# Performance work log

Measured on AMD Instinct MI355X. Metric: run time of the kernel, lower is better.

Reference implementation:

```python
import jax, jax.numpy as jnp
import numpy as np

CONF_THRESH = 0.5   # foreground objectness threshold (module default)
NMS_THRESH = 0.4    # IoU suppression threshold (module default)
SCORE_THRESH = 0.3  # hard-coded max-class-score filter in forward

BS, NUM_BOXES, NUM_ATTRS = 2, 6300, 85  # 80 classes


def setup_inputs() -> dict:
    key = jax.random.key(0)
    # uniform [0,1): boxes live in the unit square and overlap heavily,
    # objectness/class scores frequently exceed the thresholds.
    x = jax.random.uniform(key, (BS, NUM_BOXES, NUM_ATTRS), dtype=jnp.float32)
    return {"x": x}


def _nms_keep(corners, scores, cls_idx, valid):
    """Per-image, per-class greedy NMS.

    corners: [N,4] (x1,y1,x2,y2), scores: [N] objectness, cls_idx: [N] int,
    valid: [N] bool. Returns keep mask [N] bool. Faithful to the torch loop:
    sort by objectness desc, greedily keep the top box of each class and
    suppress same-class boxes with IoU >= nms_thresh (torch keeps iou < t).
    """
    n = scores.shape[0]
    order = jnp.argsort(-scores)      # descending by objectness (column 4)
    rank = jnp.argsort(order)         # rank[j] = position of box j in order

    x1, y1, x2, y2 = corners[:, 0], corners[:, 1], corners[:, 2], corners[:, 3]
    area = (x2 - x1) * (y2 - y1)
    iw = jnp.maximum(jnp.minimum(x2[:, None], x2[None, :]) -
                     jnp.maximum(x1[:, None], x1[None, :]), 0.0)
    ih = jnp.maximum(jnp.minimum(y2[:, None], y2[None, :]) -
                     jnp.maximum(y1[:, None], y1[None, :]), 0.0)
    inter = iw * ih                                   # [N,N]
    iou = inter / (area[:, None] + area[None, :] - inter + 1e-16)
    same_cls = cls_idx[:, None] == cls_idx[None, :]    # [N,N]

    def body(r, keep):
        i = order[r]
        # suppress strictly lower-ranked, still-alive, same-class overlaps
        sup = (iou[i] >= NMS_THRESH) & same_cls[i] & (rank > r)
        return jnp.where(keep[i], keep & ~sup, keep)

    return jax.lax.fori_loop(0, n, body, valid)


def reference(x):
    """x: [bs, N, 5+num_classes]. Returns detections [bs, N, 8]:
    [batch_idx, x1, y1, x2, y2, p_obj, max_cls_score, cls_idx],
    zeroed for suppressed / filtered boxes (fixed-shape analogue of the
    variable-length torch output)."""
    conf_mask = x[..., 4] > CONF_THRESH
    xm = x * conf_mask[..., None].astype(x.dtype)

    # center -> corner transform
    xy, wh = xm[..., :2], xm[..., 2:4]
    corners = jnp.concatenate([xy - wh * 0.5, xy + wh * 0.5], axis=-1)  # [bs,N,4]

    p_obj = xm[..., 4]
    cls_scores = xm[..., 5:]
    max_score = jnp.max(cls_scores, axis=-1)
    cls_idx = jnp.argmax(cls_scores, axis=-1)
    valid = conf_mask & (max_score > SCORE_THRESH)

    keep = jax.vmap(_nms_keep)(corners, p_obj, cls_idx, valid)  # [bs,N] bool

    bs, n = p_obj.shape
    batch_idx = jnp.broadcast_to(
        jnp.arange(bs, dtype=x.dtype)[:, None], (bs, n))
    det = jnp.concatenate([
        batch_idx[..., None], corners, p_obj[..., None],
        max_score[..., None], cls_idx.astype(x.dtype)[..., None]], axis=-1)
    return det * keep[..., None].astype(x.dtype)
```

## Files before the change

### kernel.cpp

```cpp
#include <hip/hip_runtime.h>

#define BSZ    2
#define NBOX   6300
#define NATTR  85
#define NCLS   80
#define NREP   8
#define RCAP   64
#define CAP    256
#define POISON 0xAAAAAAAAu
#define NCC    (BSZ * NCLS)

typedef unsigned long long ull;

static __device__ __forceinline__ ull mask_for(int rem) {
  if (rem <= 0) return 0ull;
  if (rem >= 64) return ~0ull;
  return (1ull << rem) - 1ull;
}

__global__ __launch_bounds__(256) void prep_kernel(
    const float* __restrict__ x,
    unsigned int* __restrict__ ccount,
    int* __restrict__ clist,
    float* __restrict__ out) {
  int gid  = blockIdx.x * blockDim.x + threadIdx.x;
  int box  = gid >> 6;
  int lane = threadIdx.x & 63;
  int rep  = blockIdx.x & (NREP - 1);

  const float* p = x + (long)box * NATTR;
  float r0 = p[lane];
  float r1 = (lane < NATTR - 64) ? p[64 + lane] : -1.0f;

  float c0 = (lane >= 5) ? r0 : -1.0f;
  float v; int vi;
  if (r1 > c0) { v = r1; vi = 64 + lane; }
  else         { v = c0; vi = lane; }

  for (int off = 32; off > 0; off >>= 1) {
    float ov = __shfl_xor(v, off);
    int   oi = __shfl_xor(vi, off);
    if (ov > v || (ov == v && oi < vi)) { v = ov; vi = oi; }
  }

  float cx  = __shfl(r0, 0), cy = __shfl(r0, 1);
  float bw  = __shfl(r0, 2), bh = __shfl(r0, 3);
  float obj = __shfl(r0, 4);
  bool valid = (obj > 0.5f) && (v > 0.3f);
  int  img   = box >= NBOX ? 1 : 0;
  int  cls   = vi - 5;

  if (lane == 0) {
    float4 a, b;
    if (valid) {
      float hw = bw * 0.5f, hh = bh * 0.5f;
      a = make_float4((float)img, cx - hw, cy - hh, cx + hw);
      b = make_float4(cy + hh, obj, v, (float)cls);
      int cell = rep * NCC + img * NCLS + cls;
      unsigned int pos = atomicAdd(&ccount[cell], 1u) - POISON;
      if (pos < RCAP) clist[cell * RCAP + pos] = box - img * NBOX;
    } else {
      a = make_float4(0.f, 0.f, 0.f, 0.f);
      b = a;
    }
    float4* o = (float4*)(out + (long)box * 8);
    o[0] = a; o[1] = b;
  }
}

__global__ __launch_bounds__(64) void nms_kernel(
    const unsigned int* __restrict__ ccount,
    const int* __restrict__ clist,
    float* out) {
  __shared__ float ssc[CAP];
  __shared__ int   sbi[CAP];
  __shared__ float px1[CAP], py1[CAP], px2[CAP], py2[CAP];
  __shared__ int   pbi[CAP];

  int bc   = blockIdx.x;
  int img  = bc / NCLS;
  int lane = threadIdx.x;

  int cnt[NREP], off[NREP];
  int k = 0;
#pragma unroll
  for (int r = 0; r < NREP; r++) {
    unsigned int c = ccount[r * NCC + bc] - POISON;
    int ci = c > RCAP ? RCAP : (int)c;
    off[r] = k;
    k += ci;
    cnt[r] = ci;
  }
  if (k > CAP) k = CAP;
  if (k == 0) return;

  if (k <= 64) {
    float x1 = 0.f, y1 = 0.f, x2 = 0.f, y2 = 0.f, sc = 0.f;
    int bi = 0;
    if (lane < k) {
      int src = -1;
#pragma unroll
      for (int r = 0; r < NREP; r++)
        if (lane >= off[r] && lane < off[r] + cnt[r])
          src = (r * NCC + bc) * RCAP + (lane - off[r]);
      bi = clist[src];
      const float4* o = (const float4*)(out + ((long)img * NBOX + bi) * 8);
      float4 a = o[0], b = o[1];
      x1 = a.y; y1 = a.z; x2 = a.w; y2 = b.x; sc = b.y;
    }
    int rank = 0;
    for (int i = 0; i < k; i++) {
      float si  = __shfl(sc, i);
      int   bii = __shfl(bi, i);
      rank += (si > sc) || (si == sc && bii < bi);
    }
    if (lane >= k) rank = lane;

    int r4 = rank << 2;
    x1 = __int_as_float(__builtin_amdgcn_ds_permute(r4, __float_as_int(x1)));
    y1 = __int_as_float(__builtin_amdgcn_ds_permute(r4, __float_as_int(y1)));
    x2 = __int_as_float(__builtin_amdgcn_ds_permute(r4, __float_as_int(x2)));
    y2 = __int_as_float(__builtin_amdgcn_ds_permute(r4, __float_as_int(y2)));
    bi = __builtin_amdgcn_ds_permute(r4, bi);

    float ar = (x2 - x1) * (y2 - y1);

    ull keep = mask_for(k);
    for (int r = 0; r < k - 1; r++) {
      if (!((keep >> r) & 1ull)) continue;
      float X1 = __shfl(x1, r), Y1 = __shfl(y1, r);
      float X2 = __shfl(x2, r), Y2 = __shfl(y2, r);
      float AR = __shfl(ar, r);
      float iw = fminf(X2, x2) - fmaxf(X1, x1);
      float ih = fminf(Y2, y2) - fmaxf(Y1, y1);
      iw = fmaxf(iw, 0.0f); ih = fmaxf(ih, 0.0f);
      float inter = iw * ih;
      float iou = inter / (AR + ar - inter + 1e-16f);
      keep &= ~__ballot(iou >= 0.4f && lane > r);
    }

    if (lane < k && !((keep >> lane) & 1ull)) {
      float4 z = make_float4(0.f, 0.f, 0.f, 0.f);
      float4* o = (float4*)(out + ((long)img * NBOX + bi) * 8);
      o[0] = z; o[1] = z;
    }
    return;
  }

  float gx1[4], gy1[4], gx2[4], gy2[4], gsc[4];
  int   gbi[4];
#pragma unroll
  for (int s = 0; s < 4; s++) {
    int e = s * 64 + lane;
    gx1[s] = 0; gy1[s] = 0; gx2[s] = 0; gy2[s] = 0; gsc[s] = 0; gbi[s] = 0;
    if (e < k) {
      int src = -1;
#pragma unroll
      for (int r = 0; r < NREP; r++)
        if (e >= off[r] && e < off[r] + cnt[r])
          src = (r * NCC + bc) * RCAP + (e - off[r]);
      int bi = clist[src];
      const float4* o = (const float4*)(out + ((long)img * NBOX + bi) * 8);
      float4 a = o[0], b = o[1];
      gx1[s] = a.y; gy1[s] = a.z; gx2[s] = a.w; gy2[s] = b.x; gsc[s] = b.y;
      gbi[s] = bi;
      ssc[e] = b.y; sbi[e] = bi;
    }
  }
  __syncthreads();

#pragma unroll
  for (int s = 0; s < 4; s++) {
    int e = s * 64 + lane;
    if (e < k) {
      int r = 0;
      for (int j = 0; j < k; j++) {
        float sj = ssc[j];
        r += (sj > gsc[s]) || (sj == gsc[s] && sbi[j] < gbi[s]);
      }
      px1[r] = gx1[s]; py1[r] = gy1[s];
      px2[r] = gx2[s]; py2[r] = gy2[s];
      pbi[r] = gbi[s];
    }
  }
  __syncthreads();

  float mx1[4], my1[4], mx2[4], my2[4], mar[4];
  int   mbi[4];
#pragma unroll
  for (int s = 0; s < 4; s++) {
    int e = s * 64 + lane;
    if (e < k) {
      mx1[s] = px1[e]; my1[s] = py1[e];
      mx2[s] = px2[e]; my2[s] = py2[e];
      mbi[s] = pbi[e];
      mar[s] = (mx2[s] - mx1[s]) * (my2[s] - my1[s]);
    } else {
      mx1[s] = 0; my1[s] = 0; mx2[s] = 0; my2[s] = 0; mar[s] = 0; mbi[s] = 0;
    }
  }
  ull km0 = mask_for(k);
  ull km1 = mask_for(k - 64);
  ull km2 = mask_for(k - 128);
  ull km3 = mask_for(k - 192);

  for (int r = 0; r < k - 1; r++) {
    ull cur = (r < 64) ? km0 : (r < 128) ? km1 : (r < 192) ? km2 : km3;
    if (!((cur >> (r & 63)) & 1ull)) continue;
    float X1 = px1[r], Y1 = py1[r], X2 = px2[r], Y2 = py2[r];
    float ar = (X2 - X1) * (Y2 - Y1);
    {
      int e = lane;
      float iw = fminf(X2, mx2[0]) - fmaxf(X1, mx1[0]);
      float ih = fminf(Y2, my2[0]) - fmaxf(Y1, my1[0]);
      iw = fmaxf(iw, 0.0f); ih = fmaxf(ih, 0.0f);
      float inter = iw * ih;
      float iou = inter / (ar + mar[0] - inter + 1e-16f);
      km0 &= ~__ballot(iou >= 0.4f && e > r && e < k);
    }
    if (k > 64) {
      int e = 64 + lane;
      float iw = fminf(X2, mx2[1]) - fmaxf(X1, mx1[1]);
      float ih = fminf(Y2, my2[1]) - fmaxf(Y1, my1[1]);
      iw = fmaxf(iw, 0.0f); ih = fmaxf(ih, 0.0f);
      float inter = iw * ih;
      float iou = inter / (ar + mar[1] - inter + 1e-16f);
      km1 &= ~__ballot(iou >= 0.4f && e > r && e < k);
    }
    if (k > 128) {
      int e = 128 + lane;
      float iw = fminf(X2, mx2[2]) - fmaxf(X1, mx1[2]);
      float ih = fminf(Y2, my2[2]) - fmaxf(Y1, my1[2]);
      iw = fmaxf(iw, 0.0f); ih = fmaxf(ih, 0.0f);
      float inter = iw * ih;
      float iou = inter / (ar + mar[2] - inter + 1e-16f);
      km2 &= ~__ballot(iou >= 0.4f && e > r && e < k);
    }
    if (k > 192) {
      int e = 192 + lane;
      float iw = fminf(X2, mx2[3]) - fmaxf(X1, mx1[3]);
      float ih = fminf(Y2, my2[3]) - fmaxf(Y1, my1[3]);
      iw = fmaxf(iw, 0.0f); ih = fmaxf(ih, 0.0f);
      float inter = iw * ih;
      float iou = inter / (ar + mar[3] - inter + 1e-16f);
      km3 &= ~__ballot(iou >= 0.4f && e > r && e < k);
    }
  }

  float4 z = make_float4(0.f, 0.f, 0.f, 0.f);
#pragma unroll
  for (int s = 0; s < 4; s++) {
    ull kms = (s == 0) ? km0 : (s == 1) ? km1 : (s == 2) ? km2 : km3;
    int e = s * 64 + lane;
    if (e < k && !((kms >> lane) & 1ull)) {
      float4* o = (float4*)(out + ((long)img * NBOX + mbi[s]) * 8);
      o[0] = z; o[1] = z;
    }
  }
}

extern "C" void kernel_launch(void* const* d_in, const int* in_sizes, int n_in,
                              void* d_out, int out_size, void* d_ws, size_t ws_size,
                              hipStream_t stream) {
  const float* x = (const float*)d_in[0];
  float* out = (float*)d_out;
  unsigned int* ccount = (unsigned int*)d_ws;
  int* clist = (int*)(ccount + NREP * NCC);

  prep_kernel<<<(BSZ * NBOX * 64) / 256, 256, 0, stream>>>(x, ccount, clist, out);
  nms_kernel<<<BSZ * NCLS, 64, 0, stream>>>(ccount, clist, out);
}
```

Measured before the change: 70.54 us.

## Fuse prep and NMS into one persistent kernel with a grid-wide barrier

Merges the decode/bucketing kernel and the per-class NMS kernel into one 160-block launch. An atomic counter spin-wait acts as a grid barrier between the two phases. Bucket records now carry the box coordinates and score directly, so NMS no longer gathers from the output buffer. The large-k rank computation is spread over 1024 threads instead of one wavefront. This removes a kernel launch and an indirect gather, but relies on all 160 blocks being co-resident and on the done counter starting at the poison value. It also serialises decode over fewer, larger blocks.

```diff
diff --git a/kernel.cpp b/kernel.cpp
--- a/kernel.cpp
+++ b/kernel.cpp
@@ -2,13 +2,19 @@
 
 #define BSZ    2
 #define NBOX   6300
+#define TOT    (BSZ * NBOX)
 #define NATTR  85
 #define NCLS   80
+#define NCC    (BSZ * NCLS)
 #define NREP   8
 #define RCAP   64
 #define CAP    256
 #define POISON 0xAAAAAAAAu
-#define NCC    (BSZ * NCLS)
+#define GRID   160
+#define BLK    1024
+#define WPB    16
+#define TW     (GRID * WPB)
+#define MAXIT  5
 
 typedef unsigned long long ull;
 
@@ -17,244 +23,273 @@
   if (rem >= 64) return ~0ull;
   return (1ull << rem) - 1ull;
 }
-
-__global__ __launch_bounds__(256) void prep_kernel(
+static __device__ __forceinline__ ull pkf(float lo, float hi) {
+  return (ull)__float_as_uint(lo) | ((ull)__float_as_uint(hi) << 32);
+}
+static __device__ __forceinline__ float lof(ull u) { return __uint_as_float((unsigned)u); }
+static __device__ __forceinline__ float hif(ull u) { return __uint_as_float((unsigned)(u >> 32)); }
+static __device__ __forceinline__ void st64(ull* p, ull v) {
+  __hip_atomic_store(p, v, __ATOMIC_RELAXED, __HIP_MEMORY_SCOPE_AGENT);
+}
+static __device__ __forceinline__ ull ld64(const ull* p) {
+  return __hip_atomic_load(p, __ATOMIC_RELAXED, __HIP_MEMORY_SCOPE_AGENT);
+}
+static __device__ __forceinline__ unsigned ld32(const unsigned* p) {
+  return __hip_atomic_load(p, __ATOMIC_RELAXED, __HIP_MEMORY_SCOPE_AGENT);
+}
+
+__global__ __launch_bounds__(BLK) void fused_kernel(
     const float* __restrict__ x,
-    unsigned int* __restrict__ ccount,
-    int* __restrict__ clist,
+    unsigned* __restrict__ ccount,
+    float* __restrict__ clist,
+    unsigned* __restrict__ done,
     float* __restrict__ out) {
-  int gid  = blockIdx.x * blockDim.x + threadIdx.x;
-  int box  = gid >> 6;
-  int lane = threadIdx.x & 63;
-  int rep  = blockIdx.x & (NREP - 1);
-
-  const float* p = x + (long)box * NATTR;
-  float r0 = p[lane];
-  float r1 = (lane < NATTR - 64) ? p[64 + lane] : -1.0f;
-
-  float c0 = (lane >= 5) ? r0 : -1.0f;
-  float v; int vi;
-  if (r1 > c0) { v = r1; vi = 64 + lane; }
-  else         { v = c0; vi = lane; }
-
-  for (int off = 32; off > 0; off >>= 1) {
-    float ov = __shfl_xor(v, off);
-    int   oi = __shfl_xor(vi, off);
-    if (ov > v || (ov == v && oi < vi)) { v = ov; vi = oi; }
-  }
-
-  float cx  = __shfl(r0, 0), cy = __shfl(r0, 1);
-  float bw  = __shfl(r0, 2), bh = __shfl(r0, 3);
-  float obj = __shfl(r0, 4);
-  bool valid = (obj > 0.5f) && (v > 0.3f);
-  int  img   = box >= NBOX ? 1 : 0;
-  int  cls   = vi - 5;
-
-  if (lane == 0) {
-    float4 a, b;
-    if (valid) {
-      float hw = bw * 0.5f, hh = bh * 0.5f;
-      a = make_float4((float)img, cx - hw, cy - hh, cx + hw);
-      b = make_float4(cy + hh, obj, v, (float)cls);
-      int cell = rep * NCC + img * NCLS + cls;
-      unsigned int pos = atomicAdd(&ccount[cell], 1u) - POISON;
-      if (pos < RCAP) clist[cell * RCAP + pos] = box - img * NBOX;
-    } else {
-      a = make_float4(0.f, 0.f, 0.f, 0.f);
-      b = a;
-    }
-    float4* o = (float4*)(out + (long)box * 8);
-    o[0] = a; o[1] = b;
-  }
-}
-
-__global__ __launch_bounds__(64) void nms_kernel(
-    const unsigned int* __restrict__ ccount,
-    const int* __restrict__ clist,
-    float* out) {
   __shared__ float ssc[CAP];
   __shared__ int   sbi[CAP];
   __shared__ float px1[CAP], py1[CAP], px2[CAP], py2[CAP];
   __shared__ int   pbi[CAP];
 
-  int bc   = blockIdx.x;
-  int img  = bc / NCLS;
-  int lane = threadIdx.x;
-
-  int cnt[NREP], off[NREP];
+  int t    = threadIdx.x;
+  int lane = t & 63;
+  int w    = t >> 6;
+  int b    = blockIdx.x;
+  int rep  = b & (NREP - 1);
+  int g    = b * WPB + w;
+
+  float R0[MAXIT], R1[MAXIT];
+#pragma unroll
+  for (int it = 0; it < MAXIT; it++) {
+    int box = g + it * TW;
+    if (box < TOT) {
+      const float* p = x + (long)box * NATTR;
+      R0[it] = p[lane];
+      R1[it] = (lane < NATTR - 64) ? p[64 + lane] : -1.0f;
+    } else { R0[it] = -1.0f; R1[it] = -1.0f; }
+  }
+#pragma unroll
+  for (int it = 0; it < MAXIT; it++) {
+    int box = g + it * TW;
+    if (box < TOT) {
+      float r0 = R0[it], r1 = R1[it];
+      float c0 = (lane >= 5) ? r0 : -1.0f;
+      float v; int vi;
+      if (r1 > c0) { v = r1; vi = 64 + lane; }
+      else         { v = c0; vi = lane; }
+      for (int off = 32; off > 0; off >>= 1) {
+        float ov = __shfl_xor(v, off);
+        int   oi = __shfl_xor(vi, off);
+        if (ov > v || (ov == v && oi < vi)) { v = ov; vi = oi; }
+      }
+      float cx  = __shfl(r0, 0), cy = __shfl(r0, 1);
+      float bw  = __shfl(r0, 2), bh = __shfl(r0, 3);
+      float obj = __shfl(r0, 4);
+      bool valid = (obj > 0.5f) && (v > 0.3f);
+      int  img   = box >= NBOX ? 1 : 0;
+      int  cls   = vi - 5;
+
+      if (lane == 0) {
+        ull* o = (ull*)(out + (long)box * 8);
+        if (valid) {
+          float hw = bw * 0.5f, hh = bh * 0.5f;
+          float x1 = cx - hw, y1 = cy - hh, x2 = cx + hw, y2 = cy + hh;
+          st64(o + 0, pkf((float)img, x1));
+          st64(o + 1, pkf(y1, x2));
+          st64(o + 2, pkf(y2, obj));
+          st64(o + 3, pkf(v, (float)cls));
+          int bi   = box - img * NBOX;
+          int cell = rep * NCC + img * NCLS + cls;
+          unsigned pos = atomicAdd(&ccount[cell], 1u) - POISON;
+          if (pos < RCAP) {
+            ull* rec = (ull*)(clist + ((long)cell * RCAP + pos) * 8);
+            st64(rec + 0, pkf(x1, y1));
+            st64(rec + 1, pkf(x2, y2));
+            st64(rec + 2, (ull)__float_as_uint(obj) | ((ull)(unsigned)bi << 32));
+          }
+        } else {
+          st64(o + 0, 0ull); st64(o + 1, 0ull);
+          st64(o + 2, 0ull); st64(o + 3, 0ull);
+        }
+      }
+    }
+  }
+
+  __syncthreads();
+  if (t == 0) {
+    atomicAdd(done, 1u);
+    const unsigned target = POISON + GRID;
+    while (ld32(done) != target) __builtin_amdgcn_s_sleep(2);
+  }
+  __syncthreads();
+
+  int bc  = b;
+  int img = bc / NCLS;
+
+  int cnt[NREP], offv[NREP];
   int k = 0;
 #pragma unroll
   for (int r = 0; r < NREP; r++) {
-    unsigned int c = ccount[r * NCC + bc] - POISON;
+    unsigned c = ld32(&ccount[r * NCC + bc]) - POISON;
     int ci = c > RCAP ? RCAP : (int)c;
-    off[r] = k;
-    k += ci;
-    cnt[r] = ci;
+    offv[r] = k; k += ci; cnt[r] = ci;
   }
   if (k > CAP) k = CAP;
   if (k == 0) return;
 
   if (k <= 64) {
-    float x1 = 0.f, y1 = 0.f, x2 = 0.f, y2 = 0.f, sc = 0.f;
-    int bi = 0;
-    if (lane < k) {
-      int src = -1;
-#pragma unroll
-      for (int r = 0; r < NREP; r++)
-        if (lane >= off[r] && lane < off[r] + cnt[r])
-          src = (r * NCC + bc) * RCAP + (lane - off[r]);
-      bi = clist[src];
-      const float4* o = (const float4*)(out + ((long)img * NBOX + bi) * 8);
-      float4 a = o[0], b = o[1];
-      x1 = a.y; y1 = a.z; x2 = a.w; y2 = b.x; sc = b.y;
-    }
-    int rank = 0;
-    for (int i = 0; i < k; i++) {
-      float si  = __shfl(sc, i);
-      int   bii = __shfl(bi, i);
-      rank += (si > sc) || (si == sc && bii < bi);
-    }
-    if (lane >= k) rank = lane;
-
-    int r4 = rank << 2;
-    x1 = __int_as_float(__builtin_amdgcn_ds_permute(r4, __float_as_int(x1)));
-    y1 = __int_as_float(__builtin_amdgcn_ds_permute(r4, __float_as_int(y1)));
-    x2 = __int_as_float(__builtin_amdgcn_ds_permute(r4, __float_as_int(x2)));
-    y2 = __int_as_float(__builtin_amdgcn_ds_permute(r4, __float_as_int(y2)));
-    bi = __builtin_amdgcn_ds_permute(r4, bi);
-
-    float ar = (x2 - x1) * (y2 - y1);
-
-    ull keep = mask_for(k);
+    if (w == 0) {
+      float x1 = 0.f, y1 = 0.f, x2 = 0.f, y2 = 0.f, sc = 0.f;
+      int bi = 0;
+      if (lane < k) {
+        long src = 0;
+#pragma unroll
+        for (int r = 0; r < NREP; r++)
+          if (lane >= offv[r] && lane < offv[r] + cnt[r])
+            src = ((long)(r * NCC + bc) * RCAP + (lane - offv[r])) * 8;
+        const ull* rec = (const ull*)(clist + src);
+        ull ra = ld64(rec + 0), rb = ld64(rec + 1), rc = ld64(rec + 2);
+        x1 = lof(ra); y1 = hif(ra); x2 = lof(rb); y2 = hif(rb);
+        sc = lof(rc); bi = (int)(unsigned)(rc >> 32);
+      }
+      int rank = 0;
+      for (int i = 0; i < k; i++) {
+        float si  = __shfl(sc, i);
+        int   bii = __shfl(bi, i);
+        rank += (si > sc) || (si == sc && bii < bi);
+      }
+      if (lane >= k) rank = lane;
+
+      int r4 = rank << 2;
+      x1 = __int_as_float(__builtin_amdgcn_ds_permute(r4, __float_as_int(x1)));
+      y1 = __int_as_float(__builtin_amdgcn_ds_permute(r4, __float_as_int(y1)));
+      x2 = __int_as_float(__builtin_amdgcn_ds_permute(r4, __float_as_int(x2)));
+      y2 = __int_as_float(__builtin_amdgcn_ds_permute(r4, __float_as_int(y2)));
+      bi = __builtin_amdgcn_ds_permute(r4, bi);
+
+      float ar = (x2 - x1) * (y2 - y1);
+
+      ull keep = mask_for(k);
+      for (int r = 0; r < k - 1; r++) {
+        if (!((keep >> r) & 1ull)) continue;
+        float X1 = __shfl(x1, r), Y1 = __shfl(y1, r);
+        float X2 = __shfl(x2, r), Y2 = __shfl(y2, r);
+        float AR = __shfl(ar, r);
+        float iw = fminf(X2, x2) - fmaxf(X1, x1);
+        float ih = fminf(Y2, y2) - fmaxf(Y1, y1);
+        iw = fmaxf(iw, 0.0f); ih = fmaxf(ih, 0.0f);
+        float inter = iw * ih;
+        float iou = inter / (AR + ar - inter + 1e-16f);
+        keep &= ~__ballot(iou >= 0.4f && lane > r);
+      }
+
+      if (lane < k && !((keep >> lane) & 1ull)) {
+        ull* o = (ull*)(out + ((long)img * NBOX + bi) * 8);
+        st64(o + 0, 0ull); st64(o + 1, 0ull);
+        st64(o + 2, 0ull); st64(o + 3, 0ull);
+      }
+    }
+    return;
+  }
+
+  float fx1 = 0, fy1 = 0, fx2 = 0, fy2 = 0, fsc = 0;
+  int   fbi = 0;
+  if (t < k) {
+    long src = 0;
+#pragma unroll
+    for (int r = 0; r < NREP; r++)
+      if (t >= offv[r] && t < offv[r] + cnt[r])
+        src = ((long)(r * NCC + bc) * RCAP + (t - offv[r])) * 8;
+    const ull* rec = (const ull*)(clist + src);
+    ull ra = ld64(rec + 0), rb = ld64(rec + 1), rc = ld64(rec + 2);
+    fx1 = lof(ra); fy1 = hif(ra); fx2 = lof(rb); fy2 = hif(rb);
+    fsc = lof(rc); fbi = (int)(unsigned)(rc >> 32);
+    ssc[t] = fsc; sbi[t] = fbi;
+  }
+  __syncthreads();
+
+  if (t < k) {
+    int r = 0;
+    for (int j = 0; j < k; j++) {
+      float sj = ssc[j];
+      r += (sj > fsc) || (sj == fsc && sbi[j] < fbi);
+    }
+    px1[r] = fx1; py1[r] = fy1;
+    px2[r] = fx2; py2[r] = fy2;
+    pbi[r] = fbi;
+  }
+  __syncthreads();
+
+  if (w == 0) {
+    float mx1[4], my1[4], mx2[4], my2[4], mar[4];
+    int   mbi[4];
+#pragma unroll
+    for (int s = 0; s < 4; s++) {
+      int e = s * 64 + lane;
+      if (e < k) {
+        mx1[s] = px1[e]; my1[s] = py1[e];
+        mx2[s] = px2[e]; my2[s] = py2[e];
+        mbi[s] = pbi[e];
+        mar[s] = (mx2[s] - mx1[s]) * (my2[s] - my1[s]);
+      } else {
+        mx1[s] = 0; my1[s] = 0; mx2[s] = 0; my2[s] = 0; mar[s] = 0; mbi[s] = 0;
+      }
+    }
+    ull km0 = mask_for(k);
+    ull km1 = mask_for(k - 64);
+    ull km2 = mask_for(k - 128);
+    ull km3 = mask_for(k - 192);
+
     for (int r = 0; r < k - 1; r++) {
-      if (!((keep >> r) & 1ull)) continue;
-      float X1 = __shfl(x1, r), Y1 = __shfl(y1, r);
-      float X2 = __shfl(x2, r), Y2 = __shfl(y2, r);
-      float AR = __shfl(ar, r);
-      float iw = fminf(X2, x2) - fmaxf(X1, x1);
-      float ih = fminf(Y2, y2) - fmaxf(Y1, y1);
-      iw = fmaxf(iw, 0.0f); ih = fmaxf(ih, 0.0f);
-      float inter = iw * ih;
-      float iou = inter / (AR + ar - inter + 1e-16f);
-      keep &= ~__ballot(iou >= 0.4f && lane > r);
-    }
-
-    if (lane < k && !((keep >> lane) & 1ull)) {
-      float4 z = make_float4(0.f, 0.f, 0.f, 0.f);
-      float4* o = (float4*)(out + ((long)img * NBOX + bi) * 8);
-      o[0] = z; o[1] = z;
-    }
-    return;
-  }
-
-  float gx1[4], gy1[4], gx2[4], gy2[4], gsc[4];
-  int   gbi[4];
-#pragma unroll
-  for (int s = 0; s < 4; s++) {
-    int e = s * 64 + lane;
-    gx1[s] = 0; gy1[s] = 0; gx2[s] = 0; gy2[s] = 0; gsc[s] = 0; gbi[s] = 0;
-    if (e < k) {
-      int src = -1;
-#pragma unroll
-      for (int r = 0; r < NREP; r++)
-        if (e >= off[r] && e < off[r] + cnt[r])
-          src = (r * NCC + bc) * RCAP + (e - off[r]);
-      int bi = clist[src];
-      const float4* o = (const float4*)(out + ((long)img * NBOX + bi) * 8);
-      float4 a = o[0], b = o[1];
-      gx1[s] = a.y; gy1[s] = a.z; gx2[s] = a.w; gy2[s] = b.x; gsc[s] = b.y;
-      gbi[s] = bi;
-      ssc[e] = b.y; sbi[e] = bi;
-    }
-  }
-  __syncthreads();
-
-#pragma unroll
-  for (int s = 0; s < 4; s++) {
-    int e = s * 64 + lane;
-    if (e < k) {
-      int r = 0;
-      for (int j = 0; j < k; j++) {
-        float sj = ssc[j];
-        r += (sj > gsc[s]) || (sj == gsc[s] && sbi[j] < gbi[s]);
-      }
-      px1[r] = gx1[s]; py1[r] = gy1[s];
-      px2[r] = gx2[s]; py2[r] = gy2[s];
-      pbi[r] = gbi[s];
-    }
-  }
-  __syncthreads();
-
-  float mx1[4], my1[4], mx2[4], my2[4], mar[4];
-  int   mbi[4];
-#pragma unroll
-  for (int s = 0; s < 4; s++) {
-    int e = s * 64 + lane;
-    if (e < k) {
-      mx1[s] = px1[e]; my1[s] = py1[e];
-      mx2[s] = px2[e]; my2[s] = py2[e];
-      mbi[s] = pbi[e];
-      mar[s] = (mx2[s] - mx1[s]) * (my2[s] - my1[s]);
-    } else {
-      mx1[s] = 0; my1[s] = 0; mx2[s] = 0; my2[s] = 0; mar[s] = 0; mbi[s] = 0;
-    }
-  }
-  ull km0 = mask_for(k);
-  ull km1 = mask_for(k - 64);
-  ull km2 = mask_for(k - 128);
-  ull km3 = mask_for(k - 192);
-
-  for (int r = 0; r < k - 1; r++) {
-    ull cur = (r < 64) ? km0 : (r < 128) ? km1 : (r < 192) ? km2 : km3;
-    if (!((cur >> (r & 63)) & 1ull)) continue;
-    float X1 = px1[r], Y1 = py1[r], X2 = px2[r], Y2 = py2[r];
-    float ar = (X2 - X1) * (Y2 - Y1);
-    {
-      int e = lane;
-      float iw = fminf(X2, mx2[0]) - fmaxf(X1, mx1[0]);
-      float ih = fminf(Y2, my2[0]) - fmaxf(Y1, my1[0]);
-      iw = fmaxf(iw, 0.0f); ih = fmaxf(ih, 0.0f);
-      float inter = iw * ih;
-      float iou = inter / (ar + mar[0] - inter + 1e-16f);
-      km0 &= ~__ballot(iou >= 0.4f && e > r && e < k);
-    }
-    if (k > 64) {
-      int e = 64 + lane;
-      float iw = fminf(X2, mx2[1]) - fmaxf(X1, mx1[1]);
-      float ih = fminf(Y2, my2[1]) - fmaxf(Y1, my1[1]);
-      iw = fmaxf(iw, 0.0f); ih = fmaxf(ih, 0.0f);
-      float inter = iw * ih;
-      float iou = inter / (ar + mar[1] - inter + 1e-16f);
-      km1 &= ~__ballot(iou >= 0.4f && e > r && e < k);
-    }
-    if (k > 128) {
-      int e = 128 + lane;
-      float iw = fminf(X2, mx2[2]) - fmaxf(X1, mx1[2]);
-      float ih = fminf(Y2, my2[2]) - fmaxf(Y1, my1[2]);
-      iw = fmaxf(iw, 0.0f); ih = fmaxf(ih, 0.0f);
-      float inter = iw * ih;
-      float iou = inter / (ar + mar[2] - inter + 1e-16f);
-      km2 &= ~__ballot(iou >= 0.4f && e > r && e < k);
-    }
-    if (k > 192) {
-      int e = 192 + lane;
-      float iw = fminf(X2, mx2[3]) - fmaxf(X1, mx1[3]);
-      float ih = fminf(Y2, my2[3]) - fmaxf(Y1, my1[3]);
-      iw = fmaxf(iw, 0.0f); ih = fmaxf(ih, 0.0f);
-      float inter = iw * ih;
-      float iou = inter / (ar + mar[3] - inter + 1e-16f);
-      km3 &= ~__ballot(iou >= 0.4f && e > r && e < k);
-    }
-  }
-
-  float4 z = make_float4(0.f, 0.f, 0.f, 0.f);
-#pragma unroll
-  for (int s = 0; s < 4; s++) {
-    ull kms = (s == 0) ? km0 : (s == 1) ? km1 : (s == 2) ? km2 : km3;
-    int e = s * 64 + lane;
-    if (e < k && !((kms >> lane) & 1ull)) {
-      float4* o = (float4*)(out + ((long)img * NBOX + mbi[s]) * 8);
-      o[0] = z; o[1] = z;
+      ull cur = (r < 64) ? km0 : (r < 128) ? km1 : (r < 192) ? km2 : km3;
+      if (!((cur >> (r & 63)) & 1ull)) continue;
+      float X1 = px1[r], Y1 = py1[r], X2 = px2[r], Y2 = py2[r];
+      float ar = (X2 - X1) * (Y2 - Y1);
+      {
+        int e = lane;
+        float iw = fminf(X2, mx2[0]) - fmaxf(X1, mx1[0]);
+        float ih = fminf(Y2, my2[0]) - fmaxf(Y1, my1[0]);
+        iw = fmaxf(iw, 0.0f); ih = fmaxf(ih, 0.0f);
+        float inter = iw * ih;
+        float iou = inter / (ar + mar[0] - inter + 1e-16f);
+        km0 &= ~__ballot(iou >= 0.4f && e > r && e < k);
+      }
+      if (k > 64) {
+        int e = 64 + lane;
+        float iw = fminf(X2, mx2[1]) - fmaxf(X1, mx1[1]);
+        float ih = fminf(Y2, my2[1]) - fmaxf(Y1, my1[1]);
+        iw = fmaxf(iw, 0.0f); ih = fmaxf(ih, 0.0f);
+        float inter = iw * ih;
+        float iou = inter / (ar + mar[1] - inter + 1e-16f);
+        km1 &= ~__ballot(iou >= 0.4f && e > r && e < k);
+      }
+      if (k > 128) {
+        int e = 128 + lane;
+        float iw = fminf(X2, mx2[2]) - fmaxf(X1, mx1[2]);
+        float ih = fminf(Y2, my2[2]) - fmaxf(Y1, my1[2]);
+        iw = fmaxf(iw, 0.0f); ih = fmaxf(ih, 0.0f);
+        float inter = iw * ih;
+        float iou = inter / (ar + mar[2] - inter + 1e-16f);
+        km2 &= ~__ballot(iou >= 0.4f && e > r && e < k);
+      }
+      if (k > 192) {
+        int e = 192 + lane;
+        float iw = fminf(X2, mx2[3]) - fmaxf(X1, mx1[3]);
+        float ih = fminf(Y2, my2[3]) - fmaxf(Y1, my1[3]);
+        iw = fmaxf(iw, 0.0f); ih = fmaxf(ih, 0.0f);
+        float inter = iw * ih;
+        float iou = inter / (ar + mar[3] - inter + 1e-16f);
+        km3 &= ~__ballot(iou >= 0.4f && e > r && e < k);
+      }
+    }
+
+#pragma unroll
+    for (int s = 0; s < 4; s++) {
+      ull kms = (s == 0) ? km0 : (s == 1) ? km1 : (s == 2) ? km2 : km3;
+      int e = s * 64 + lane;
+      if (e < k && !((kms >> lane) & 1ull)) {
+        ull* o = (ull*)(out + ((long)img * NBOX + mbi[s]) * 8);
+        st64(o + 0, 0ull); st64(o + 1, 0ull);
+        st64(o + 2, 0ull); st64(o + 3, 0ull);
+      }
     }
   }
 }
@@ -264,9 +299,9 @@
                               hipStream_t stream) {
   const float* x = (const float*)d_in[0];
   float* out = (float*)d_out;
-  unsigned int* ccount = (unsigned int*)d_ws;
-  int* clist = (int*)(ccount + NREP * NCC);
-
-  prep_kernel<<<(BSZ * NBOX * 64) / 256, 256, 0, stream>>>(x, ccount, clist, out);
-  nms_kernel<<<BSZ * NCLS, 64, 0, stream>>>(ccount, clist, out);
-}
+  unsigned* ccount = (unsigned*)d_ws;
+  float* clist = (float*)(ccount + NREP * NCC);
+  unsigned* done = (unsigned*)(clist + (long)NREP * NCC * RCAP * 8);
+
+  fused_kernel<<<GRID, BLK, 0, stream>>>(x, ccount, clist, done, out);
+}
```

Result: slower. 76.52 us (+8.5%).
